# Kernel optimization log

Hardware: AMD Instinct MI355X
Metric: run time of the kernel (lower is better)

Reference implementation:

```python
import jax, jax.numpy as jnp
import numpy as np

TOPK = 16  # matches selected per (frame, query pixel)


def setup_inputs() -> dict:
    key = jax.random.key(0)
    ks = jax.random.split(key, 4)
    B, T, N, C = 2, 3, 4096, 256  # batch, ref frames, 64x64 tokens, channels
    scale = 1.0 / np.sqrt(C)
    return {
        "tgt": jax.random.normal(ks[0], (B, N, C), dtype=jnp.float32),
        "ref": jax.random.normal(ks[1], (B, T, N, C), dtype=jnp.float32),
        "Wq": jax.random.normal(ks[2], (C, C), dtype=jnp.float32) * scale,
        "bq": jnp.zeros((C,), dtype=jnp.float32),
        "Wk": jax.random.normal(ks[3], (C, C), dtype=jnp.float32) * scale,
        "bk": jnp.zeros((C,), dtype=jnp.float32),
    }


def _l2norm(x, eps=1e-12):
    return x * jax.lax.rsqrt(jnp.sum(x * x, axis=-1, keepdims=True) + eps)


def reference(tgt, ref, Wq, bq, Wk, bk):
    # tgt: [B, Nq, C] target-frame tokens; ref: [B, T, Nr, C] reference-frame tokens
    B, Nq, C = tgt.shape
    T, Nr = ref.shape[1], ref.shape[2]
    q = _l2norm(tgt @ Wq + bq)                      # [B, Nq, C]
    k = _l2norm(ref @ Wk + bk)                      # [B, T, Nr, C]
    # cross-frame cosine-similarity correlation volume
    sim = jnp.einsum("bqc,btrc->btqr", q, k)        # [B, T, Nq, Nr]
    # top-k matched reference locations per query pixel
    topv, topi = jax.lax.top_k(sim, TOPK)           # [B, T, Nq, K]
    # gather matched reference features (irregular gather)
    bi = jnp.arange(B)[:, None, None, None]
    ti = jnp.arange(T)[None, :, None, None]
    gathered = ref[bi, ti, topi]                    # [B, T, Nq, K, C]
    # attention-weighted aggregation of matched features
    w = jax.nn.softmax(topv, axis=-1)               # [B, T, Nq, K]
    out = jnp.einsum("btqk,btqkc->btqc", w, gathered)  # [B, T, Nq, C]
    return out
```

## Files before the change

### kernel.cpp

```cpp
#include <hip/hip_runtime.h>
#include <hip/hip_fp16.h>
#include <stdint.h>
#include <math.h>

#define T_FRAMES 3
#define NTOK 4096
#define CH 256

typedef __attribute__((ext_vector_type(8))) short bf16x8;
typedef __attribute__((ext_vector_type(4))) float f32x4;
typedef __attribute__((ext_vector_type(4))) double f64x4;
typedef __attribute__((address_space(1))) void gvoid;
typedef __attribute__((address_space(3))) void svoid;

__device__ __forceinline__ unsigned short f2bf_rne(float f) {
  union { float f; uint32_t u; } c; c.f = f;
  uint32_t u = c.u;
  return (unsigned short)((u + 0x7FFFu + ((u >> 16) & 1u)) >> 16);
}
__device__ __forceinline__ float bflo(uint32_t x) { return __uint_as_float(x << 16); }
__device__ __forceinline__ float bfhi(uint32_t x) { return __uint_as_float(x & 0xFFFF0000u); }

__device__ __forceinline__ int dec_class(double v, int* idx) {
  const double t0 = (v - 96.0) * 0.25;
  const double t1 = (v - 6.0) * 0.0625;
  if (t0 >= 0.0 && t0 <= 15.0 && t0 == floor(t0)) { *idx = (int)t0; return 0; }
  if (t1 >= 0.0 && t1 <= 15.0 && t1 == floor(t1)) { *idx = (int)t1; return 1; }
  return -1;
}

__global__ __launch_bounds__(64) void probe_kernel(int* map) {
  __shared__ int cover[256];
  const int l = threadIdx.x;
  #pragma unroll
  for (int i = 0; i < 4; i++) cover[l + i * 64] = 0;
  __syncthreads();
  const f64x4 z = {0.0, 0.0, 0.0, 0.0};
  const f64x4 d1 = __builtin_amdgcn_mfma_f64_16x16x4f64(1.0, (double)l, z, 0, 0, 0);
  const f64x4 d2 = __builtin_amdgcn_mfma_f64_16x16x4f64((double)l, 1.0, z, 0, 0, 0);
  int ok = 1, cls0 = -1, cls1 = -1;
  int alpha[4], beta[4];
  #pragma unroll
  for (int r = 0; r < 4; r++) {
    int idx;
    int c = dec_class(d1[r], &idx);
    if (r == 0) cls1 = c;
    ok &= (c >= 0) & (c == cls1);
    beta[r] = (c >= 0) ? idx : 0;
    c = dec_class(d2[r], &idx);
    if (r == 0) cls0 = c;
    ok &= (c >= 0) & (c == cls0);
    alpha[r] = (c >= 0) ? idx : 0;
  }
  ok &= (cls0 == __shfl(cls0, 0));
  ok &= (cls1 == __shfl(cls1, 0));
  #pragma unroll
  for (int r = 0; r < 4; r++) atomicAdd(&cover[alpha[r] * 16 + beta[r]], 1);
  __syncthreads();
  #pragma unroll
  for (int i = 0; i < 4; i++) ok &= (cover[l + i * 64] == 1);
  if (cls0 >= 0 && cls1 >= 0) {
    const int k0 = (cls0 == 0) ? (l >> 4) : (l & 3);
    const int k1 = (cls1 == 0) ? (l >> 4) : (l & 3);
    const double a0v = (k0 == 0) ? 1.0 : ((k0 == 1) ? 5.0 : ((k0 == 2) ? 25.0 : 125.0));
    const f64x4 d3 = __builtin_amdgcn_mfma_f64_16x16x4f64(a0v, (double)k1, z, 0, 0, 0);
    #pragma unroll
    for (int r = 0; r < 4; r++) ok &= (d3[r] == 430.0);
  } else {
    ok = 0;
  }
  ok = __all(ok) ? 1 : 0;
  if (l == 0) { map[0] = ok; map[1] = cls0; map[2] = cls1; }
  #pragma unroll
  for (int r = 0; r < 4; r++) {
    map[16 + l * 4 + r]  = alpha[r];
    map[272 + l * 4 + r] = beta[r];
  }
}

__global__ __launch_bounds__(256) void proj_mfma_kernel(
    const float* __restrict__ Xq, const float* __restrict__ Wq, const float* __restrict__ bq,
    const float* __restrict__ Xk, const float* __restrict__ Wk, const float* __restrict__ bk,
    unsigned short* __restrict__ Qb, float* __restrict__ Qlo,
    unsigned short* __restrict__ Kb, float* __restrict__ Klo,
    const int* __restrict__ map)
{
  if (map[0] != 1) return;
  __shared__ double ssArr[16][65];
  const int tid = threadIdx.x;
  const int wv = tid >> 6, l = tid & 63;
  int blk = blockIdx.x;
  const float *X, *W, *bias; unsigned short* Pb; float* Plo;
  if (blk < 512) { X = Xq; W = Wq; bias = bq; Pb = Qb; Plo = Qlo; }
  else           { X = Xk; W = Wk; bias = bk; Pb = Kb; Plo = Klo; blk -= 512; }
  const int rbase = blk * 16;
  const int cls0 = map[1], cls1 = map[2];
  int alpha[4], beta[4];
  #pragma unroll
  for (int r = 0; r < 4; r++) {
    alpha[r] = map[16 + l * 4 + r];
    beta[r]  = map[272 + l * 4 + r];
  }
  const int a0 = (cls0 == 0) ? (l & 15) : (l >> 2);
  const int k0 = (cls0 == 0) ? (l >> 4) : (l & 3);
  const int b1 = (cls1 == 0) ? (l & 15) : (l >> 2);
  const int k1 = (cls1 == 0) ? (l >> 4) : (l & 3);
  const int ctb = wv * 4;

  f64x4 acc[4];
  #pragma unroll
  for (int c = 0; c < 4; c++) {
    #pragma unroll
    for (int r = 0; r < 4; r++) acc[c][r] = (double)bias[(ctb + c) * 16 + beta[r]];
  }

  const float* xp = X + (size_t)(rbase + a0) * CH + k0;
  const float* wp = W + (size_t)k1 * CH + ctb * 16 + b1;
  for (int kc = 0; kc < 64; kc++) {
    const double ad = (double)xp[kc * 4];
    const float* wrow = wp + (size_t)(kc * 4) * CH;
    #pragma unroll
    for (int c = 0; c < 4; c++)
      acc[c] = __builtin_amdgcn_mfma_f64_16x16x4f64(ad, (double)wrow[c * 16], acc[c], 0, 0, 0);
  }

  #pragma unroll
  for (int r = 0; r < 4; r++) {
    double part = 0.0;
    #pragma unroll
    for (int c = 0; c < 4; c++) part += acc[c][r] * acc[c][r];
    ssArr[alpha[r]][wv * 16 + beta[r]] = part;
  }
  __syncthreads();
  #pragma unroll
  for (int r = 0; r < 4; r++) {
    const int rw = alpha[r];
    double ss = 0.0;
    #pragma unroll 8
    for (int j = 0; j < 64; j++) ss += ssArr[rw][j];
    const double inv = 1.0 / sqrt(ss + 1e-12);
    #pragma unroll
    for (int c = 0; c < 4; c++) {
      const double vd = acc[c][r] * inv;
      const unsigned short us = f2bf_rne((float)vd);
      const float fb = __uint_as_float(((uint32_t)us) << 16);
      const size_t idx = (size_t)(rbase + rw) * CH + (ctb + c) * 16 + beta[r];
      Pb[idx] = us;
      Plo[idx] = (float)(vd - (double)fb);
    }
  }
}

__global__ __launch_bounds__(256) void proj_valu_kernel(
    const float* __restrict__ Xq, const float* __restrict__ Wq, const float* __restrict__ bq,
    const float* __restrict__ Xk, const float* __restrict__ Wk, const float* __restrict__ bk,
    unsigned short* __restrict__ Qb, float* __restrict__ Qlo,
    unsigned short* __restrict__ Kb, float* __restrict__ Klo,
    const int* __restrict__ map)
{
  if (map[0] == 1) return;
  __shared__ double At[4][64][8];
  const int tid = threadIdx.x;
  int blk = blockIdx.x;
  const float *X, *W, *bias; unsigned short* Pb; float* Plo;
  if (blk < 256) { X = Xq; W = Wq; bias = bq; Pb = Qb; Plo = Qlo; }
  else           { X = Xk; W = Wk; bias = bk; Pb = Kb; Plo = Klo; blk -= 256; }
  const int rbase = blk * 32;
  const int wv = tid >> 6, lane = tid & 63;
  const int r0 = wv * 8;
  const int c4 = lane * 4;

  double acc[8][4];
  #pragma unroll
  for (int i = 0; i < 8; i++) {
    #pragma unroll
    for (int j = 0; j < 4; j++) acc[i][j] = (double)bias[c4 + j];
  }

  const int srow_l = lane & 7;
  const int skq = (lane >> 3) * 8;
  const float* xrow = X + (size_t)(rbase + r0 + srow_l) * CH + skq;

  for (int kc = 0; kc < CH; kc += 64) {
    {
      const float4 v0 = *(const float4*)(xrow + kc);
      const float4 v1 = *(const float4*)(xrow + kc + 4);
      At[wv][skq + 0][srow_l] = (double)v0.x; At[wv][skq + 1][srow_l] = (double)v0.y;
      At[wv][skq + 2][srow_l] = (double)v0.z; At[wv][skq + 3][srow_l] = (double)v0.w;
      At[wv][skq + 4][srow_l] = (double)v1.x; At[wv][skq + 5][srow_l] = (double)v1.y;
      At[wv][skq + 6][srow_l] = (double)v1.z; At[wv][skq + 7][srow_l] = (double)v1.w;
    }
    #pragma unroll 8
    for (int k = 0; k < 64; k++) {
      const float4 w4 = *(const float4*)(W + (size_t)(kc + k) * CH + c4);
      const double b0 = (double)w4.x, b1 = (double)w4.y;
      const double b2 = (double)w4.z, b3 = (double)w4.w;
      double a[8];
      #pragma unroll
      for (int i = 0; i < 4; i++) {
        const double2 ap = *(const double2*)&At[wv][k][2 * i];
        a[2*i] = ap.x; a[2*i+1] = ap.y;
      }
      #pragma unroll
      for (int i = 0; i < 8; i++) {
        acc[i][0] += a[i] * b0; acc[i][1] += a[i] * b1;
        acc[i][2] += a[i] * b2; acc[i][3] += a[i] * b3;
      }
    }
  }

  #pragma unroll
  for (int i = 0; i < 8; i++) {
    double ss = acc[i][0]*acc[i][0] + acc[i][1]*acc[i][1]
              + acc[i][2]*acc[i][2] + acc[i][3]*acc[i][3];
    #pragma unroll
    for (int off = 32; off >= 1; off >>= 1) ss += __shfl_xor(ss, off);
    const double inv = 1.0 / sqrt(ss + 1e-12);
    const size_t base = (size_t)(rbase + r0 + i) * CH + c4;
    double vd[4]; float fb[4]; unsigned short us[4];
    #pragma unroll
    for (int j = 0; j < 4; j++) {
      vd[j] = acc[i][j] * inv;
      us[j] = f2bf_rne((float)vd[j]);
      fb[j] = __uint_as_float(((uint32_t)us[j]) << 16);
    }
    uint2 pk; pk.x = (uint32_t)us[0] | ((uint32_t)us[1] << 16);
    pk.y = (uint32_t)us[2] | ((uint32_t)us[3] << 16);
    *(uint2*)(Pb + base) = pk;
    float4 lo;
    lo.x = (float)(vd[0] - (double)fb[0]); lo.y = (float)(vd[1] - (double)fb[1]);
    lo.z = (float)(vd[2] - (double)fb[2]); lo.w = (float)(vd[3] - (double)fb[3]);
    *(float4*)(Plo + base) = lo;
  }
}

__global__ __launch_bounds__(256, 4) void sim_cand_kernel(
    const unsigned short* __restrict__ Qb,
    const unsigned short* __restrict__ Kb,
    uint32_t* __restrict__ cand,
    const float* __restrict__ ref,
    unsigned short* __restrict__ ref16, int use16)
{
  __shared__ unsigned short kst[2][32 * 256];
  const int bid = blockIdx.x;
  const int rs = bid & 3;
  const int qb = (bid >> 2) & 63;
  const int bt = bid >> 8;
  const int b = bt / T_FRAMES;
  const int tid = threadIdx.x;
  const int wv = tid >> 6, lane = tid & 63;
  const int lq = lane & 15, g = lane >> 4;
  const int q = qb * 64 + wv * 16 + lq;

  if (use16) {
    #pragma unroll
    for (int pass = 0; pass < 2; pass++) {
      const size_t i = (size_t)bid * 4096 + (size_t)pass * 2048 + (size_t)tid * 8;
      const float4 v0 = *(const float4*)(ref + i);
      const float4 v1 = *(const float4*)(ref + i + 4);
      const uint32_t h0 = (uint32_t)__half_as_ushort(__float2half_rn(v0.x));
      const uint32_t h1 = (uint32_t)__half_as_ushort(__float2half_rn(v0.y));
      const uint32_t h2 = (uint32_t)__half_as_ushort(__float2half_rn(v0.z));
      const uint32_t h3 = (uint32_t)__half_as_ushort(__float2half_rn(v0.w));
      const uint32_t h4 = (uint32_t)__half_as_ushort(__float2half_rn(v1.x));
      const uint32_t h5 = (uint32_t)__half_as_ushort(__float2half_rn(v1.y));
      const uint32_t h6 = (uint32_t)__half_as_ushort(__float2half_rn(v1.z));
      const uint32_t h7 = (uint32_t)__half_as_ushort(__float2half_rn(v1.w));
      uint4 hv;
      hv.x = h0 | (h1 << 16); hv.y = h2 | (h3 << 16);
      hv.z = h4 | (h5 << 16); hv.w = h6 | (h7 << 16);
      *(uint4*)(ref16 + i) = hv;
    }
  }

  bf16x8 bfr[8];
  {
    const unsigned short* qrow = Qb + (size_t)(b * NTOK + q) * CH + g * 8;
    #pragma unroll
    for (int kc = 0; kc < 8; kc++) bfr[kc] = *(const bf16x8*)(qrow + kc * 32);
  }
  uint32_t best[16];
  #pragma unroll
  for (int i = 0; i < 16; i++) best[i] = 0u;
  uint32_t s[16];

  const unsigned short* kbase = Kb + ((size_t)bt * NTOK + (size_t)rs * 1024) * CH;

#define STAGE(C, BUFI)                                                          \
  {                                                                             \
    _Pragma("unroll")                                                           \
    for (int t = 0; t < 4; t++) {                                               \
      const int o16 = (wv * 4 + t) * 64 + lane;                                 \
      const int row = o16 >> 5, colp = o16 & 31;                                \
      const int col16 = (colp - row) & 31;                                      \
      const unsigned short* gsrc = kbase + (size_t)((C) * 32 + row) * CH + col16 * 8; \
      __builtin_amdgcn_global_load_lds((const gvoid*)gsrc,                      \
          (svoid*)(&kst[BUFI][0] + (size_t)(wv * 4 + t) * 512), 16, 0, 0);      \
    }                                                                           \
  }

#define COMPUTE_HALF(CBASE, BUFI, SOFF)                                         \
  {                                                                             \
    _Pragma("unroll")                                                           \
    for (int t = 0; t < 2; t++) {                                               \
      f32x4 acc = {2.0f, 2.0f, 2.0f, 2.0f};                                     \
      const int arow = t * 16 + lq;                                             \
      const unsigned short* rowp = &kst[BUFI][0] + (size_t)arow * 256;          \
      _Pragma("unroll")                                                         \
      for (int kc = 0; kc < 8; kc++) {                                          \
        const int colp = (kc * 4 + g + arow) & 31;                              \
        const bf16x8 a = *(const bf16x8*)(rowp + colp * 8);                     \
        acc = __builtin_amdgcn_mfma_f32_16x16x32_bf16(a, bfr[kc], acc, 0, 0, 0);\
      }                                                                         \
      _Pragma("unroll")                                                         \
      for (int j = 0; j < 4; j++) {                                             \
        const uint32_t bits = __float_as_uint(acc[j]);                          \
        s[(SOFF) + t * 4 + j] = (bits & 0xFFFFFC00u) |                          \
            (uint32_t)((CBASE) * 32 + t * 16 + g * 4 + j);                      \
      }                                                                         \
    }                                                                           \
  }

#define SORT16_MERGE()                                                          \
  {                                                                             \
    _Pragma("unroll")                                                           \
    for (int bk = 2; bk <= 16; bk <<= 1) {                                      \
      _Pragma("unroll")                                                         \
      for (int bj = bk >> 1; bj > 0; bj >>= 1) {                                \
        _Pragma("unroll")                                                       \
        for (int i = 0; i < 16; i++) {                                          \
          const int l = i ^ bj;                                                 \
          if (l > i) {                                                          \
            const bool up = ((i & bk) != 0);                                    \
            const uint32_t a2 = s[i], b2 = s[l];                                \
            const uint32_t mn = a2 < b2 ? a2 : b2;                              \
            const uint32_t mx = a2 < b2 ? b2 : a2;                              \
            s[i] = up ? mn : mx; s[l] = up ? mx : mn;                           \
          }                                                                     \
        }                                                                       \
      }                                                                         \
    }                                                                           \
    uint32_t m[16];                                                             \
    _Pragma("unroll")                                                           \
    for (int i = 0; i < 16; i++) {                                              \
      const uint32_t a2 = best[i], b2 = s[15 - i];                              \
      m[i] = a2 > b2 ? a2 : b2;                                                 \
    }                                                                           \
    _Pragma("unroll")                                                           \
    for (int bj = 8; bj > 0; bj >>= 1) {                                        \
      _Pragma("unroll")                                                         \
      for (int i = 0; i < 16; i++) {                                            \
        const int l = i ^ bj;                                                   \
        if (l > i) {                                                            \
          const uint32_t a2 = m[i], b2 = m[l];                                  \
          const uint32_t mn = a2 < b2 ? a2 : b2;                                \
          const uint32_t mx = a2 < b2 ? b2 : a2;                                \
          m[i] = mx; m[l] = mn;                                                 \
        }                                                                       \
      }                                                                         \
    }                                                                           \
    _Pragma("unroll")                                                           \
    for (int i = 0; i < 16; i++) best[i] = m[i];                                \
  }

  STAGE(0, 0);
  __syncthreads();
  for (int cp = 0; cp < 16; cp++) {
    const int c0 = 2 * cp;
    STAGE(c0 + 1, 1);
    COMPUTE_HALF(c0, 0, 0);
    __syncthreads();
    if (cp < 15) STAGE(c0 + 2, 0);
    COMPUTE_HALF(c0 + 1, 1, 8);
    SORT16_MERGE();
    __syncthreads();
  }

  #pragma unroll
  for (int st = 16; st <= 32; st <<= 1) {
    uint32_t o[16];
    #pragma unroll
    for (int i = 0; i < 16; i++) o[i] = (uint32_t)__shfl_xor((int)best[15 - i], st);
    #pragma unroll
    for (int i = 0; i < 16; i++) best[i] = best[i] > o[i] ? best[i] : o[i];
    #pragma unroll
    for (int bj = 8; bj > 0; bj >>= 1) {
      #pragma unroll
      for (int i = 0; i < 16; i++) {
        const int l = i ^ bj;
        if (l > i) {
          const uint32_t a2 = best[i], b2 = best[l];
          const uint32_t mn = a2 < b2 ? a2 : b2;
          const uint32_t mx = a2 < b2 ? b2 : a2;
          best[i] = mx; best[l] = mn;
        }
      }
    }
  }
  if (g == 0) {
    uint32_t* cp2 = cand + ((size_t)bt * NTOK + q) * 64 + rs * 16;
    #pragma unroll
    for (int i = 0; i < 16; i += 4) {
      uint4 v; v.x = best[i]; v.y = best[i+1]; v.z = best[i+2]; v.w = best[i+3];
      *(uint4*)(cp2 + i) = v;
    }
  }
#undef STAGE
#undef COMPUTE_HALF
#undef SORT16_MERGE
}

__global__ __launch_bounds__(256) void out_kernel(
    const unsigned short* __restrict__ Qb, const float* __restrict__ Qlo,
    const unsigned short* __restrict__ Kb, const float* __restrict__ Klo,
    const uint32_t* __restrict__ cand, const float* __restrict__ ref,
    const unsigned short* __restrict__ ref16, int use16,
    float* __restrict__ out)
{
  const int tid = threadIdx.x, wv = tid >> 6, lane = tid & 63;
  const int bid = blockIdx.x;
  const int work = (bid & 7) * 768 + (bid >> 3);
  const int rowid = work * 4 + wv;
  const int bt = rowid >> 12, q = rowid & 4095;
  const int b = bt / T_FRAMES;

  const uint32_t k0 = cand[(size_t)rowid * 64 + lane];
  uint32_t key = (k0 & 0xFFFFF000u) | ((uint32_t)(lane >> 4) << 10) | (k0 & 0x3FFu);

  #pragma unroll
  for (int k = 2; k <= 64; k <<= 1) {
    #pragma unroll
    for (int j = k >> 1; j > 0; j >>= 1) {
      const uint32_t ok = (uint32_t)__shfl_xor((int)key, j);
      const bool takeMax = (((lane & j) != 0) == ((lane & k) == 0));
      if ((ok > key) == takeMax) key = ok;
    }
  }
  const float v = __uint_as_float(key & 0xFFFFF000u) - 2.0f;
  int rr = (int)(key & 0xFFFu);

  const float v16c = __shfl(v, 48);
  const float BW = 2.5e-3f;
  const bool band = fabsf(v - v16c) <= BW;

  const uint2 qbv = *(const uint2*)(Qb + (size_t)(b * NTOK + q) * CH + lane * 4);
  const float4 qlv = *(const float4*)(Qlo + (size_t)(b * NTOK + q) * CH + lane * 4);
  const double qd0 = (double)bflo(qbv.x) + (double)qlv.x;
  const double qd1 = (double)bfhi(qbv.x) + (double)qlv.y;
  const double qd2 = (double)bflo(qbv.y) + (double)qlv.z;
  const double qd3 = (double)bfhi(qbv.y) + (double)qlv.w;

  const unsigned short* kbp = Kb + (size_t)bt * NTOK * CH;
  const float* klp = Klo + (size_t)bt * NTOK * CH;

  double dval = -1.0e300;
  {
    const unsigned long long bm = __ballot(band);
    const int lo = __ffsll(bm) - 1;
    const int hi = 63 - __clzll(bm);
    for (int idx = lo; idx <= hi; idx++) {
      const int ri = __shfl(rr, idx);
      const uint2 kbv = *(const uint2*)(kbp + (size_t)ri * CH + lane * 4);
      const float4 klv = *(const float4*)(klp + (size_t)ri * CH + lane * 4);
      double dd = qd0 * ((double)bflo(kbv.x) + (double)klv.x)
                + qd1 * ((double)bfhi(kbv.x) + (double)klv.y)
                + qd2 * ((double)bflo(kbv.y) + (double)klv.z)
                + qd3 * ((double)bfhi(kbv.y) + (double)klv.w);
      #pragma unroll
      for (int off = 32; off >= 1; off >>= 1) dd += __shfl_xor(dd, off);
      if (lane == idx) dval = dd;
    }
  }
  double p = band ? dval : ((v > v16c + BW) ? (double)v : -1.0e300);

  #pragma unroll
  for (int k = 2; k <= 64; k <<= 1) {
    #pragma unroll
    for (int j = k >> 1; j > 0; j >>= 1) {
      const double op = __shfl_xor(p, j);
      const int orr = __shfl_xor(rr, j);
      const bool takeMax = (((lane & j) != 0) == ((lane & k) == 0));
      const bool og = (op > p) || (op == p && orr < rr);
      if (takeMax == og) { p = op; rr = orr; }
    }
  }

  double pm = p;
  #pragma unroll
  for (int j = 8; j >= 1; j >>= 1) pm = fmax(pm, __shfl_xor(pm, j));
  double e = (lane >= 48) ? exp(p - pm) : 0.0;
  double es = e;
  #pragma unroll
  for (int j = 8; j >= 1; j >>= 1) es += __shfl_xor(es, j);
  const float w = (float)(e / es);

  float a0 = 0.f, a1 = 0.f, a2 = 0.f, a3 = 0.f;
  if (use16) {
    const unsigned short* rb16 = ref16 + (size_t)bt * NTOK * CH + lane * 4;
    #pragma unroll
    for (int i = 0; i < 16; i++) {
      const float wi = __shfl(w, 48 + i);
      const int ri = __shfl(rr, 48 + i) & 0xFFF;
      const uint2 hv = *(const uint2*)(rb16 + (size_t)ri * CH);
      a0 += wi * __half2float(__ushort_as_half((unsigned short)(hv.x & 0xFFFFu)));
      a1 += wi * __half2float(__ushort_as_half((unsigned short)(hv.x >> 16)));
      a2 += wi * __half2float(__ushort_as_half((unsigned short)(hv.y & 0xFFFFu)));
      a3 += wi * __half2float(__ushort_as_half((unsigned short)(hv.y >> 16)));
    }
  } else {
    const float* rbp = ref + (size_t)bt * NTOK * CH + lane * 4;
    #pragma unroll
    for (int i = 0; i < 16; i++) {
      const float wi = __shfl(w, 48 + i);
      const int ri = __shfl(rr, 48 + i) & 0xFFF;
      const float4 f = *(const float4*)(rbp + (size_t)ri * CH);
      a0 += wi * f.x; a1 += wi * f.y; a2 += wi * f.z; a3 += wi * f.w;
    }
  }
  float4 o; o.x = a0; o.y = a1; o.z = a2; o.w = a3;
  *(float4*)(out + (size_t)rowid * CH + lane * 4) = o;
}

extern "C" void kernel_launch(void* const* d_in, const int* in_sizes, int n_in,
                              void* d_out, int out_size, void* d_ws, size_t ws_size,
                              hipStream_t stream) {
  const float* tgt = (const float*)d_in[0];
  const float* ref = (const float*)d_in[1];
  const float* Wq  = (const float*)d_in[2];
  const float* bq  = (const float*)d_in[3];
  const float* Wk  = (const float*)d_in[4];
  const float* bk  = (const float*)d_in[5];
  float* out = (float*)d_out;

  const int B = 2;
  const int RQ = B * NTOK;
  const int RK = B * T_FRAMES * NTOK;

  char* ws = (char*)d_ws;
  unsigned short* Qb = (unsigned short*)ws; ws += (size_t)RQ * CH * 2;
  float* Qlo = (float*)ws;                  ws += (size_t)RQ * CH * 4;
  unsigned short* Kb = (unsigned short*)ws; ws += (size_t)RK * CH * 2;
  float* Klo = (float*)ws;                  ws += (size_t)RK * CH * 4;
  uint32_t* cand = (uint32_t*)ws;           ws += (size_t)RK * 64 * 4;
  const bool big = ws_size >= (size_t)69206016;
  unsigned short* ref16 = big ? (unsigned short*)ws : nullptr;
  const int use16 = big ? 1 : 0;

  int* map = (int*)cand;

  probe_kernel<<<1, 64, 0, stream>>>(map);
  proj_mfma_kernel<<<RQ / 16 + RK / 16, 256, 0, stream>>>(
      tgt, Wq, bq, ref, Wk, bk, Qb, Qlo, Kb, Klo, map);
  proj_valu_kernel<<<RQ / 32 + RK / 32, 256, 0, stream>>>(
      tgt, Wq, bq, ref, Wk, bk, Qb, Qlo, Kb, Klo, map);
  sim_cand_kernel<<<6 * 64 * 4, 256, 0, stream>>>(Qb, Kb, cand, ref, ref16, use16);
  out_kernel<<<RK / 4, 256, 0, stream>>>(Qb, Qlo, Kb, Klo, cand, ref, ref16, use16, out);
}
```

Baseline: 250.8 us.

## Split projection rows between FP64 VALU and FP64 MFMA paths in one kernel

```diff
diff --git a/kernel.cpp b/kernel.cpp
--- a/kernel.cpp
+++ b/kernel.cpp
@@ -78,7 +78,7 @@
   }
 }
 
-__global__ __launch_bounds__(256) void proj_mfma_kernel(
+__global__ __launch_bounds__(256) void proj_dual_kernel(
     const float* __restrict__ Xq, const float* __restrict__ Wq, const float* __restrict__ bq,
     const float* __restrict__ Xk, const float* __restrict__ Wk, const float* __restrict__ bk,
     unsigned short* __restrict__ Qb, float* __restrict__ Qlo,
@@ -86,67 +86,145 @@
     const int* __restrict__ map)
 {
   if (map[0] != 1) return;
-  __shared__ double ssArr[16][65];
+  __shared__ double shmem[2048];
   const int tid = threadIdx.x;
-  const int wv = tid >> 6, l = tid & 63;
-  int blk = blockIdx.x;
-  const float *X, *W, *bias; unsigned short* Pb; float* Plo;
-  if (blk < 512) { X = Xq; W = Wq; bias = bq; Pb = Qb; Plo = Qlo; }
-  else           { X = Xk; W = Wk; bias = bk; Pb = Kb; Plo = Klo; blk -= 512; }
-  const int rbase = blk * 16;
-  const int cls0 = map[1], cls1 = map[2];
-  int alpha[4], beta[4];
-  #pragma unroll
-  for (int r = 0; r < 4; r++) {
-    alpha[r] = map[16 + l * 4 + r];
-    beta[r]  = map[272 + l * 4 + r];
-  }
-  const int a0 = (cls0 == 0) ? (l & 15) : (l >> 2);
-  const int k0 = (cls0 == 0) ? (l >> 4) : (l & 3);
-  const int b1 = (cls1 == 0) ? (l & 15) : (l >> 2);
-  const int k1 = (cls1 == 0) ? (l >> 4) : (l & 3);
-  const int ctb = wv * 4;
-
-  f64x4 acc[4];
-  #pragma unroll
-  for (int c = 0; c < 4; c++) {
-    #pragma unroll
-    for (int r = 0; r < 4; r++) acc[c][r] = (double)bias[(ctb + c) * 16 + beta[r]];
-  }
-
-  const float* xp = X + (size_t)(rbase + a0) * CH + k0;
-  const float* wp = W + (size_t)k1 * CH + ctb * 16 + b1;
-  for (int kc = 0; kc < 64; kc++) {
-    const double ad = (double)xp[kc * 4];
-    const float* wrow = wp + (size_t)(kc * 4) * CH;
-    #pragma unroll
-    for (int c = 0; c < 4; c++)
-      acc[c] = __builtin_amdgcn_mfma_f64_16x16x4f64(ad, (double)wrow[c * 16], acc[c], 0, 0, 0);
-  }
-
-  #pragma unroll
-  for (int r = 0; r < 4; r++) {
-    double part = 0.0;
-    #pragma unroll
-    for (int c = 0; c < 4; c++) part += acc[c][r] * acc[c][r];
-    ssArr[alpha[r]][wv * 16 + beta[r]] = part;
-  }
-  __syncthreads();
-  #pragma unroll
-  for (int r = 0; r < 4; r++) {
-    const int rw = alpha[r];
-    double ss = 0.0;
-    #pragma unroll 8
-    for (int j = 0; j < 64; j++) ss += ssArr[rw][j];
-    const double inv = 1.0 / sqrt(ss + 1e-12);
+  const int bid = blockIdx.x;
+  const int r3 = bid % 3;
+
+  if (r3 == 0) {
+    double (*At)[64][8] = (double(*)[64][8])shmem;
+    int v = bid / 3;
+    const float *X, *W, *bias; unsigned short* Pb; float* Plo;
+    int rbase;
+    if (v < 256) { X = Xq; W = Wq; bias = bq; Pb = Qb; Plo = Qlo; rbase = v * 32; }
+    else         { X = Xk; W = Wk; bias = bk; Pb = Kb; Plo = Klo; rbase = (v - 256) * 32; }
+    const int wv = tid >> 6, lane = tid & 63;
+    const int r0 = wv * 8;
+    const int c4 = lane * 4;
+
+    double acc[8][4];
+    #pragma unroll
+    for (int i = 0; i < 8; i++) {
+      #pragma unroll
+      for (int j = 0; j < 4; j++) acc[i][j] = (double)bias[c4 + j];
+    }
+
+    const int srow_l = lane & 7;
+    const int skq = (lane >> 3) * 8;
+    const float* xrow = X + (size_t)(rbase + r0 + srow_l) * CH + skq;
+
+    for (int kc = 0; kc < CH; kc += 64) {
+      {
+        const float4 v0 = *(const float4*)(xrow + kc);
+        const float4 v1 = *(const float4*)(xrow + kc + 4);
+        At[wv][skq + 0][srow_l] = (double)v0.x; At[wv][skq + 1][srow_l] = (double)v0.y;
+        At[wv][skq + 2][srow_l] = (double)v0.z; At[wv][skq + 3][srow_l] = (double)v0.w;
+        At[wv][skq + 4][srow_l] = (double)v1.x; At[wv][skq + 5][srow_l] = (double)v1.y;
+        At[wv][skq + 6][srow_l] = (double)v1.z; At[wv][skq + 7][srow_l] = (double)v1.w;
+      }
+      #pragma unroll 8
+      for (int k = 0; k < 64; k++) {
+        const float4 w4 = *(const float4*)(W + (size_t)(kc + k) * CH + c4);
+        const double b0 = (double)w4.x, b1 = (double)w4.y;
+        const double b2 = (double)w4.z, b3 = (double)w4.w;
+        double a[8];
+        #pragma unroll
+        for (int i = 0; i < 4; i++) {
+          const double2 ap = *(const double2*)&At[wv][k][2 * i];
+          a[2*i] = ap.x; a[2*i+1] = ap.y;
+        }
+        #pragma unroll
+        for (int i = 0; i < 8; i++) {
+          acc[i][0] += a[i] * b0; acc[i][1] += a[i] * b1;
+          acc[i][2] += a[i] * b2; acc[i][3] += a[i] * b3;
+        }
+      }
+    }
+
+    #pragma unroll
+    for (int i = 0; i < 8; i++) {
+      double ss = acc[i][0]*acc[i][0] + acc[i][1]*acc[i][1]
+                + acc[i][2]*acc[i][2] + acc[i][3]*acc[i][3];
+      #pragma unroll
+      for (int off = 32; off >= 1; off >>= 1) ss += __shfl_xor(ss, off);
+      const double inv = 1.0 / sqrt(ss + 1e-12);
+      const size_t base = (size_t)(rbase + r0 + i) * CH + c4;
+      double vd[4]; float fb[4]; unsigned short us[4];
+      #pragma unroll
+      for (int j = 0; j < 4; j++) {
+        vd[j] = acc[i][j] * inv;
+        us[j] = f2bf_rne((float)vd[j]);
+        fb[j] = __uint_as_float(((uint32_t)us[j]) << 16);
+      }
+      uint2 pk; pk.x = (uint32_t)us[0] | ((uint32_t)us[1] << 16);
+      pk.y = (uint32_t)us[2] | ((uint32_t)us[3] << 16);
+      *(uint2*)(Pb + base) = pk;
+      float4 lo;
+      lo.x = (float)(vd[0] - (double)fb[0]); lo.y = (float)(vd[1] - (double)fb[1]);
+      lo.z = (float)(vd[2] - (double)fb[2]); lo.w = (float)(vd[3] - (double)fb[3]);
+      *(float4*)(Plo + base) = lo;
+    }
+  } else {
+    double (*ssArr)[65] = (double(*)[65])shmem;
+    const int mblk = (bid / 3) * 2 + (r3 - 1);
+    const float* X = Xk; const float* W = Wk; const float* bias = bk;
+    unsigned short* Pb = Kb; float* Plo = Klo;
+    const int rbase = 8192 + mblk * 16;
+    const int wv = tid >> 6, l = tid & 63;
+    const int cls0 = map[1], cls1 = map[2];
+    int alpha[4], beta[4];
+    #pragma unroll
+    for (int r = 0; r < 4; r++) {
+      alpha[r] = map[16 + l * 4 + r];
+      beta[r]  = map[272 + l * 4 + r];
+    }
+    const int a0 = (cls0 == 0) ? (l & 15) : (l >> 2);
+    const int k0 = (cls0 == 0) ? (l >> 4) : (l & 3);
+    const int b1 = (cls1 == 0) ? (l & 15) : (l >> 2);
+    const int k1 = (cls1 == 0) ? (l >> 4) : (l & 3);
+    const int ctb = wv * 4;
+
+    f64x4 acc[4];
     #pragma unroll
     for (int c = 0; c < 4; c++) {
-      const double vd = acc[c][r] * inv;
-      const unsigned short us = f2bf_rne((float)vd);
-      const float fb = __uint_as_float(((uint32_t)us) << 16);
-      const size_t idx = (size_t)(rbase + rw) * CH + (ctb + c) * 16 + beta[r];
-      Pb[idx] = us;
-      Plo[idx] = (float)(vd - (double)fb);
+      #pragma unroll
+      for (int r = 0; r < 4; r++) acc[c][r] = (double)bias[(ctb + c) * 16 + beta[r]];
+    }
+
+    const float* xp = X + (size_t)(rbase + a0) * CH + k0;
+    const float* wp = W + (size_t)k1 * CH + ctb * 16 + b1;
+    for (int kc = 0; kc < 64; kc++) {
+      const double ad = (double)xp[kc * 4];
+      const float* wrow = wp + (size_t)(kc * 4) * CH;
+      #pragma unroll
+      for (int c = 0; c < 4; c++)
+        acc[c] = __builtin_amdgcn_mfma_f64_16x16x4f64(ad, (double)wrow[c * 16], acc[c], 0, 0, 0);
+    }
+
+    #pragma unroll
+    for (int r = 0; r < 4; r++) {
+      double part = 0.0;
+      #pragma unroll
+      for (int c = 0; c < 4; c++) part += acc[c][r] * acc[c][r];
+      ssArr[alpha[r]][wv * 16 + beta[r]] = part;
+    }
+    __syncthreads();
+    #pragma unroll
+    for (int r = 0; r < 4; r++) {
+      const int rw = alpha[r];
+      double ss = 0.0;
+      #pragma unroll 8
+      for (int j = 0; j < 64; j++) ss += ssArr[rw][j];
+      const double inv = 1.0 / sqrt(ss + 1e-12);
+      #pragma unroll
+      for (int c = 0; c < 4; c++) {
+        const double vd = acc[c][r] * inv;
+        const unsigned short us = f2bf_rne((float)vd);
+        const float fb = __uint_as_float(((uint32_t)us) << 16);
+        const size_t idx = (size_t)(rbase + rw) * CH + (ctb + c) * 16 + beta[r];
+        Pb[idx] = us;
+        Plo[idx] = (float)(vd - (double)fb);
+      }
     }
   }
 }
@@ -549,7 +627,7 @@
   int* map = (int*)cand;
 
   probe_kernel<<<1, 64, 0, stream>>>(map);
-  proj_mfma_kernel<<<RQ / 16 + RK / 16, 256, 0, stream>>>(
+  proj_dual_kernel<<<1536, 256, 0, stream>>>(
       tgt, Wq, bq, ref, Wk, bk, Qb, Qlo, Kb, Klo, map);
   proj_valu_kernel<<<RQ / 32 + RK / 32, 256, 0, stream>>>(
       tgt, Wq, bq, ref, Wk, bk, Qb, Qlo, Kb, Klo, map);
```

After: 281.7 us. 1.12x slower.
